# Kernel optimization log

Measured on AMD Instinct MI355X. Metric: run time of the kernel, lower is better.

## Reference

```python
import jax, jax.numpy as jnp
import numpy as np
import math

N_HEADS = 8
NUM_LAYERS = 2
OUT_LEN = 96
MIN_FACTOR, MAX_FACTOR = 3, 10
MIN_KERNEL, MAX_KERNEL = 5, 51
LN_EPS = 1e-5


def layer_norm(x, g, b):
    mu = x.mean(-1, keepdims=True)
    var = x.var(-1, keepdims=True)  # biased, like nn.LayerNorm
    return (x - mu) / jnp.sqrt(var + LN_EPS) * g + b


def prob_sparse_attn(x, wq, bq, wk, bk, wv, bv, wo, bo):
    B, L, D = x.shape
    H, dk = N_HEADS, D // N_HEADS
    Q = (x @ wq + bq).reshape(B, L, H, dk).transpose(0, 2, 1, 3)  # [B,H,L,dk]
    K = (x @ wk + bk).reshape(B, L, H, dk).transpose(0, 2, 1, 3)
    V = (x @ wv + bv).reshape(B, L, H, dk).transpose(0, 2, 1, 3)
    # sparsity score per query: 0.5*||q|| + 0.3*entropy(softmax(q)) + 0.2*var(q)
    l2 = jnp.linalg.norm(Q, axis=-1)
    prob = jax.nn.softmax(Q, axis=-1)
    ent = -jnp.sum(prob * jnp.log(prob + 1e-9), axis=-1)
    var = Q.var(axis=-1, ddof=1)  # torch.var unbiased
    qs = 0.5 * l2 + 0.3 * ent + 0.2 * var  # [B,H,L]
    std = qs.std(axis=2, ddof=1)
    mean = qs.mean(axis=2)
    factor = jnp.clip(jnp.round(std / (mean + 1e-6) * MAX_FACTOR), MIN_FACTOR, MAX_FACTOR).astype(jnp.int32)  # [B,H]
    u = factor[:, 0]  # torch uses k_list[b][0]: head-0 factor per batch
    umax = min(MAX_FACTOR, L)
    _, top_idx = jax.lax.top_k(qs, umax)  # [B,H,umax]
    keep = jnp.arange(umax)[None, None, :] < u[:, None, None]  # [B,1->H,umax]
    Qs = jnp.take_along_axis(Q, top_idx[..., None], axis=2)  # [B,H,umax,dk]
    scores = jnp.einsum('bhud,bhld->bhul', Qs, K) / math.sqrt(dk)
    attn = jax.nn.softmax(scores, axis=-1)
    out = jnp.einsum('bhul,bhld->bhud', attn, V)  # [B,H,umax,dk]
    # scatter selected query outputs back; rows beyond u[b] are dropped (OOB index L)
    idx = jnp.where(keep, top_idx, L)
    full = jnp.zeros((B, H, L, dk), x.dtype)
    bI = jnp.arange(B)[:, None, None]
    hI = jnp.arange(H)[None, :, None]
    full = full.at[bI, hI, idx].set(out, mode='drop')
    y = full.transpose(0, 2, 1, 3).reshape(B, L, D)
    return y @ wo + bo


def adaptive_decomp(x):
    B, L, D = x.shape
    spec = jnp.abs(jnp.fft.rfft(x, axis=1)).mean(axis=(0, 2))
    peak = jnp.argmax(spec[1:]) + 1
    period = jnp.clip(L // peak, MIN_KERNEL, MAX_KERNEL)
    period = jnp.where(period % 2 == 0, period + 1, period)
    pad = period // 2
    # avg_pool1d(kernel=period, stride=1, padding=pad, count_include_pad=False) via cumsum
    t = jnp.arange(L)
    start = jnp.clip(t - pad, 0, L)
    end = jnp.clip(t + pad + 1, 0, L)
    cs = jnp.concatenate([jnp.zeros((B, 1, D), x.dtype), jnp.cumsum(x, axis=1)], axis=1)
    cnt = (end - start).astype(x.dtype)[None, :, None]
    trend = (cs[:, end] - cs[:, start]) / cnt
    return x - trend, trend


def _forward(x, w_embed, b_embed, wq, bq, wk, bk, wv, bv, wo, bo,
             w1, b1, w2, b2, g1, beta1, g2, beta2, w_out, b_out):
    h = x @ w_embed + b_embed
    for _ in range(NUM_LAYERS):  # share_params=True: same weights each layer
        a = prob_sparse_attn(h, wq, bq, wk, bk, wv, bv, wo, bo)
        h = layer_norm(h + a, g1, beta1)
        ffn = jax.nn.relu(h @ w1 + b1) @ w2 + b2
        h = layer_norm(h + ffn, g2, beta2)
    seasonal, trend = adaptive_decomp(h)
    combined = seasonal + trend
    out_seq = combined[:, -OUT_LEN:, :]
    pred = (out_seq @ w_out + b_out)[..., 0]  # [B, OUT_LEN]
    return pred


def setup_inputs() -> dict:
    key = jax.random.key(0)
    ks = jax.random.split(key, 16)
    B, L, Din, D, Dff = 16, 4096, 8, 512, 2048
    w = lambda k, shp: (jax.random.normal(k, shp, jnp.float32) * 0.02)
    return {
        'x': jax.random.normal(ks[0], (B, L, Din), jnp.float32),
        'w_embed': w(ks[1], (Din, D)), 'b_embed': jnp.zeros((D,), jnp.float32),
        'wq': w(ks[2], (D, D)), 'bq': jnp.zeros((D,), jnp.float32),
        'wk': w(ks[3], (D, D)), 'bk': jnp.zeros((D,), jnp.float32),
        'wv': w(ks[4], (D, D)), 'bv': jnp.zeros((D,), jnp.float32),
        'wo': w(ks[5], (D, D)), 'bo': jnp.zeros((D,), jnp.float32),
        'w1': w(ks[6], (D, Dff)), 'b1': jnp.zeros((Dff,), jnp.float32),
        'w2': w(ks[7], (Dff, D)), 'b2': jnp.zeros((D,), jnp.float32),
        'g1': jnp.ones((D,), jnp.float32), 'beta1': jnp.zeros((D,), jnp.float32),
        'g2': jnp.ones((D,), jnp.float32), 'beta2': jnp.zeros((D,), jnp.float32),
        'w_out': w(ks[8], (D, 1)), 'b_out': jnp.zeros((1,), jnp.float32),
    }


def reference(x, w_embed, b_embed, wq, bq, wk, bk, wv, bv, wo, bo,
              w1, b1, w2, b2, g1, beta1, g2, beta2, w_out, b_out):
    return _forward(x, w_embed, b_embed, wq, bq, wk, bk, wv, bv, wo, bo,
                    w1, b1, w2, b2, g1, beta1, g2, beta2, w_out, b_out)
```

## Files before the change

kernel.cpp:

```cpp
#include <hip/hip_runtime.h>
#include <math.h>

#define BB 16
#define LL 4096
#define DIN 8
#define DD 512
#define HH 8
#define DKK 64
#define DFF 2048
#define OUTLEN 96
#define TAIL0 (LL - OUTLEN)
#define NTAIL (BB * OUTLEN)
#define UMAX 10
#define CH 8192
#define QKVN 1536
#define NB 4
#define QM (NB * LL)
#define NSPLIT 32
#define LCHUNK (LL / NSPLIT)
#define PSTRIDE 68
#define MAXSLOT 128
#define EROWS 16

typedef unsigned short ushort_t;
typedef unsigned int uint_t;
typedef short bf16x8 __attribute__((ext_vector_type(8)));
typedef float f32x4 __attribute__((ext_vector_type(4)));

#define GLD16(gp, lp) __builtin_amdgcn_global_load_lds((const __attribute__((address_space(1))) void*)(gp), (__attribute__((address_space(3))) void*)(lp), 16, 0, 0)

__device__ inline float wsum(float v){
#pragma unroll
  for (int o = 32; o > 0; o >>= 1) v += __shfl_xor(v, o);
  return v;
}
__device__ inline ushort_t f2bf_rtn(float f){
  uint_t u = __float_as_uint(f);
  uint_t r = u + 0x7FFF + ((u >> 16) & 1);
  return (ushort_t)(r >> 16);
}
__device__ inline float bf2f(ushort_t u){
  return __uint_as_float(((uint_t)u) << 16);
}
__device__ inline void split2(float x, ushort_t& hi, ushort_t& lo){
  uint_t u = __float_as_uint(x);
  hi = (ushort_t)(u >> 16);
  lo = f2bf_rtn(x - __uint_as_float(u & 0xFFFF0000u));
}
__device__ inline void xcd_map(int& bx, int& by){
  const int gx = gridDim.x;
  const int nwg = gx * gridDim.y;
  const int wg = (int)blockIdx.y * gx + (int)blockIdx.x;
  const int q = nwg >> 3, r = nwg & 7;
  const int xcd = wg & 7, idx = wg >> 3;
  const int swz = (xcd < r ? xcd * (q + 1) : r * (q + 1) + (xcd - r) * q) + idx;
  bx = swz % gx; by = swz / gx;
}

__global__ __launch_bounds__(256) void embed_kernel(const float* __restrict__ x,
    const float* __restrict__ we, const float* __restrict__ be,
    ushort_t* __restrict__ hh, ushort_t* __restrict__ hl){
  const int row0 = blockIdx.x * EROWS;
  __shared__ float xs[EROWS][DIN];
  const int t = threadIdx.x;
  if (t < EROWS * DIN) xs[t >> 3][t & 7] = x[(size_t)row0 * DIN + t];
  __syncthreads();
  const int j0 = 2 * t;
  float w0[DIN], w1r[DIN];
#pragma unroll
  for (int i = 0; i < DIN; ++i){ w0[i] = we[i * DD + j0]; w1r[i] = we[i * DD + j0 + 1]; }
  const float b0 = be[j0], b1 = be[j0 + 1];
#pragma unroll
  for (int rr = 0; rr < EROWS; ++rr){
    float a0 = b0, a1 = b1;
#pragma unroll
    for (int i = 0; i < DIN; ++i){ a0 += xs[rr][i] * w0[i]; a1 += xs[rr][i] * w1r[i]; }
    ushort_t h0, l0, h1, l1;
    split2(a0, h0, l0); split2(a1, h1, l1);
    ((uint_t*)(hh + (size_t)(row0 + rr) * DD))[t] = (uint_t)h0 | ((uint_t)h1 << 16);
    ((uint_t*)(hl + (size_t)(row0 + rr) * DD))[t] = (uint_t)l0 | ((uint_t)l1 << 16);
  }
}

__global__ __launch_bounds__(256) void wsplit_t_kernel(const float* __restrict__ W,
    ushort_t* __restrict__ Th, ushort_t* __restrict__ Tl, int K, int N){
  __shared__ float tile[32][33];
  const int n0 = blockIdx.x * 32;
  const int k0 = blockIdx.y * 32;
  const int tr = threadIdx.x >> 5;
  const int tc = threadIdx.x & 31;
#pragma unroll
  for (int rr = 0; rr < 4; ++rr)
    tile[tr + rr * 8][tc] = W[(size_t)(k0 + tr + rr * 8) * N + n0 + tc];
  __syncthreads();
#pragma unroll
  for (int rr = 0; rr < 4; ++rr){
    const int n = n0 + tr + rr * 8;
    ushort_t hi, lo;
    split2(tile[tc][tr + rr * 8], hi, lo);
    Th[(size_t)n * K + k0 + tc] = hi;
    Tl[(size_t)n * K + k0 + tc] = lo;
  }
}
__global__ __launch_bounds__(256) void wqkv_prep_kernel(const float* __restrict__ wq,
    const float* __restrict__ wk, const float* __restrict__ wv,
    ushort_t* __restrict__ Th, ushort_t* __restrict__ Tl){
  __shared__ float tile[32][33];
  const int n0 = blockIdx.x * 32;
  const int k0 = blockIdx.y * 32;
  const float* src = (n0 < 512) ? wq : (n0 < 1024) ? wk : wv;
  const int nb = n0 & 511;
  const int tr = threadIdx.x >> 5;
  const int tc = threadIdx.x & 31;
#pragma unroll
  for (int rr = 0; rr < 4; ++rr)
    tile[tr + rr * 8][tc] = src[(size_t)(k0 + tr + rr * 8) * DD + nb + tc];
  __syncthreads();
#pragma unroll
  for (int rr = 0; rr < 4; ++rr){
    const int n = n0 + tr + rr * 8;
    ushort_t hi, lo;
    split2(tile[tc][tr + rr * 8], hi, lo);
    Th[(size_t)n * DD + k0 + tc] = hi;
    Tl[(size_t)n * DD + k0 + tc] = lo;
  }
}
__global__ __launch_bounds__(256) void bqkv_prep_kernel(const float* __restrict__ bq,
    const float* __restrict__ bk, const float* __restrict__ bv, float* __restrict__ bo_){
  int n = blockIdx.x * 256 + threadIdx.x;
  if (n >= QKVN) return;
  bo_[n] = (n < 512) ? bq[n] : (n < 1024) ? bk[n - 512] : bv[n - 1024];
}

__global__ __launch_bounds__(256) void gemm_qkv(
    const ushort_t* __restrict__ Ah, const ushort_t* __restrict__ Al,
    const ushort_t* __restrict__ Bh, const ushort_t* __restrict__ Bl,
    const float* __restrict__ bias, float* __restrict__ Q,
    ushort_t* __restrict__ KV){
  __shared__ __align__(16) ushort_t AsH[128 * 32];
  __shared__ __align__(16) ushort_t AsL[128 * 32];
  __shared__ __align__(16) ushort_t BsH[128 * 32];
  __shared__ __align__(16) ushort_t BsL[128 * 32];
  int bx, by; xcd_map(bx, by);
  const int tid  = threadIdx.x;
  const int lane = tid & 63;
  const int wv   = tid >> 6;
  const int m0   = by * 128;
  const int n0   = bx * 128;
  const bool isQ = (n0 < 512);
  const int wm   = (wv & 1) * 64;
  const int wn   = (wv >> 1) * 64;

  const int rowA = tid >> 2;
  const int qe   = (tid & 3) * 8;
  const int lds0 = tid * 8;
  const int lds1 = (tid + 256) * 8;

  f32x4 acc[4][4];
#pragma unroll
  for (int i = 0; i < 4; ++i)
#pragma unroll
    for (int j = 0; j < 4; ++j) acc[i][j] = (f32x4){0.f, 0.f, 0.f, 0.f};

  const int arow = lane & 15;
  const int koff = (lane >> 4) * 8;
  const int K = DD;

  for (int k0 = 0; k0 < K; k0 += 32){
    const size_t ga0 = (size_t)(m0 + rowA) * K + k0 + qe;
    const size_t ga1 = (size_t)(m0 + rowA + 64) * K + k0 + qe;
    const size_t gb0 = (size_t)(n0 + rowA) * K + k0 + qe;
    const size_t gb1 = (size_t)(n0 + rowA + 64) * K + k0 + qe;
    GLD16(Ah + ga0, &AsH[lds0]);  GLD16(Ah + ga1, &AsH[lds1]);
    GLD16(Al + ga0, &AsL[lds0]);  GLD16(Al + ga1, &AsL[lds1]);
    GLD16(Bh + gb0, &BsH[lds0]);  GLD16(Bh + gb1, &BsH[lds1]);
    if (isQ){ GLD16(Bl + gb0, &BsL[lds0]);  GLD16(Bl + gb1, &BsL[lds1]); }
    __syncthreads();

    bf16x8 ah[4], al[4], bh[4], bl[4];
#pragma unroll
    for (int i = 0; i < 4; ++i){
      ah[i] = *(const bf16x8*)&AsH[(wm + i * 16 + arow) * 32 + koff];
      al[i] = *(const bf16x8*)&AsL[(wm + i * 16 + arow) * 32 + koff];
      bh[i] = *(const bf16x8*)&BsH[(wn + i * 16 + arow) * 32 + koff];
      if (isQ) bl[i] = *(const bf16x8*)&BsL[(wn + i * 16 + arow) * 32 + koff];
    }
#pragma unroll
    for (int i = 0; i < 4; ++i)
#pragma unroll
      for (int j = 0; j < 4; ++j){
        acc[i][j] = __builtin_amdgcn_mfma_f32_16x16x32_bf16(ah[i], bh[j], acc[i][j], 0, 0, 0);
        acc[i][j] = __builtin_amdgcn_mfma_f32_16x16x32_bf16(al[i], bh[j], acc[i][j], 0, 0, 0);
        if (isQ)
          acc[i][j] = __builtin_amdgcn_mfma_f32_16x16x32_bf16(ah[i], bl[j], acc[i][j], 0, 0, 0);
      }
    __syncthreads();
  }

  const int crow = (lane >> 4) * 4;
  const int ccol = lane & 15;
#pragma unroll
  for (int i = 0; i < 4; ++i){
    const int gr0 = m0 + wm + i * 16 + crow;
#pragma unroll
    for (int j = 0; j < 4; ++j){
      const int gc = n0 + wn + j * 16 + ccol;
      const float bvv = bias[gc];
#pragma unroll
      for (int r = 0; r < 4; ++r){
        float v = acc[i][j][r] + bvv;
        const int gr = gr0 + r;
        if (isQ) Q[(size_t)gr * 512 + gc] = v;
        else     KV[(size_t)gr * 1024 + (gc - 512)] = f2bf_rtn(v);
      }
    }
  }
}

__global__ __launch_bounds__(256) void gemm_ffn1(
    const ushort_t* __restrict__ Ah, const ushort_t* __restrict__ Al,
    const ushort_t* __restrict__ Bh, const float* __restrict__ bias,
    ushort_t* __restrict__ Chid){
  __shared__ __align__(16) ushort_t AsH[128 * 32];
  __shared__ __align__(16) ushort_t AsL[128 * 32];
  __shared__ __align__(16) ushort_t BsH[128 * 32];
  int bx, by; xcd_map(bx, by);
  const int tid  = threadIdx.x;
  const int lane = tid & 63;
  const int wv   = tid >> 6;
  const int m0   = by * 128;
  const int n0   = bx * 128;
  const int wm   = (wv & 1) * 64;
  const int wn   = (wv >> 1) * 64;
  const int rowA = tid >> 2;
  const int qe   = (tid & 3) * 8;
  const int lds0 = tid * 8;
  const int lds1 = (tid + 256) * 8;

  f32x4 acc[4][4];
#pragma unroll
  for (int i = 0; i < 4; ++i)
#pragma unroll
    for (int j = 0; j < 4; ++j) acc[i][j] = (f32x4){0.f, 0.f, 0.f, 0.f};

  const int arow = lane & 15;
  const int koff = (lane >> 4) * 8;
  const int K = DD;

  for (int k0 = 0; k0 < K; k0 += 32){
    const size_t ga0 = (size_t)(m0 + rowA) * K + k0 + qe;
    const size_t ga1 = (size_t)(m0 + rowA + 64) * K + k0 + qe;
    const size_t gb0 = (size_t)(n0 + rowA) * K + k0 + qe;
    const size_t gb1 = (size_t)(n0 + rowA + 64) * K + k0 + qe;
    GLD16(Ah + ga0, &AsH[lds0]);  GLD16(Ah + ga1, &AsH[lds1]);
    GLD16(Al + ga0, &AsL[lds0]);  GLD16(Al + ga1, &AsL[lds1]);
    GLD16(Bh + gb0, &BsH[lds0]);  GLD16(Bh + gb1, &BsH[lds1]);
    __syncthreads();

    bf16x8 ah[4], al[4], bh[4];
#pragma unroll
    for (int i = 0; i < 4; ++i){
      ah[i] = *(const bf16x8*)&AsH[(wm + i * 16 + arow) * 32 + koff];
      al[i] = *(const bf16x8*)&AsL[(wm + i * 16 + arow) * 32 + koff];
      bh[i] = *(const bf16x8*)&BsH[(wn + i * 16 + arow) * 32 + koff];
    }
#pragma unroll
    for (int i = 0; i < 4; ++i)
#pragma unroll
      for (int j = 0; j < 4; ++j){
        acc[i][j] = __builtin_amdgcn_mfma_f32_16x16x32_bf16(ah[i], bh[j], acc[i][j], 0, 0, 0);
        acc[i][j] = __builtin_amdgcn_mfma_f32_16x16x32_bf16(al[i], bh[j], acc[i][j], 0, 0, 0);
      }
    __syncthreads();
  }

  const int crow = (lane >> 4) * 4;
  const int ccol = lane & 15;
#pragma unroll
  for (int i = 0; i < 4; ++i){
    const int gr0 = m0 + wm + i * 16 + crow;
#pragma unroll
    for (int j = 0; j < 4; ++j){
      const int gc = n0 + wn + j * 16 + ccol;
      const float bvv = bias[gc];
#pragma unroll
      for (int r = 0; r < 4; ++r){
        float v = fmaxf(acc[i][j][r] + bvv, 0.f);
        Chid[(size_t)(gr0 + r) * DFF + gc] = f2bf_rtn(v);
      }
    }
  }
}

__global__ __launch_bounds__(256) void gemm_ffn2(
    const ushort_t* __restrict__ Ahid,
    const ushort_t* __restrict__ Bh, const ushort_t* __restrict__ Bl,
    float* __restrict__ pbuf, size_t pstr){
  __shared__ __align__(16) ushort_t AsH[128 * 32];
  __shared__ __align__(16) ushort_t BsH[128 * 32];
  __shared__ __align__(16) ushort_t BsL[128 * 32];
  int bx, by; xcd_map(bx, by);
  const int tid  = threadIdx.x;
  const int lane = tid & 63;
  const int wv   = tid >> 6;
  const int nblk = bx >> 1;
  const int kq   = bx & 1;
  const int m0   = by * 128;
  const int n0   = nblk * 128;
  const int wm   = (wv & 1) * 64;
  const int wn   = (wv >> 1) * 64;
  const int rowA = tid >> 2;
  const int qe   = (tid & 3) * 8;
  const int lds0 = tid * 8;
  const int lds1 = (tid + 256) * 8;

  f32x4 acc[4][4];
#pragma unroll
  for (int i = 0; i < 4; ++i)
#pragma unroll
    for (int j = 0; j < 4; ++j) acc[i][j] = (f32x4){0.f, 0.f, 0.f, 0.f};

  const int arow = lane & 15;
  const int koff = (lane >> 4) * 8;
  const int K = DFF;
  const int kper = K / 2;
  const int kbeg = kq * kper;

  for (int k0 = kbeg; k0 < kbeg + kper; k0 += 32){
    const size_t ga0 = (size_t)(m0 + rowA) * K + k0 + qe;
    const size_t ga1 = (size_t)(m0 + rowA + 64) * K + k0 + qe;
    const size_t gb0 = (size_t)(n0 + rowA) * K + k0 + qe;
    const size_t gb1 = (size_t)(n0 + rowA + 64) * K + k0 + qe;
    GLD16(Ahid + ga0, &AsH[lds0]);  GLD16(Ahid + ga1, &AsH[lds1]);
    GLD16(Bh + gb0, &BsH[lds0]);    GLD16(Bh + gb1, &BsH[lds1]);
    GLD16(Bl + gb0, &BsL[lds0]);    GLD16(Bl + gb1, &BsL[lds1]);
    __syncthreads();

    bf16x8 ah[4], bh[4], bl[4];
#pragma unroll
    for (int i = 0; i < 4; ++i){
      ah[i] = *(const bf16x8*)&AsH[(wm + i * 16 + arow) * 32 + koff];
      bh[i] = *(const bf16x8*)&BsH[(wn + i * 16 + arow) * 32 + koff];
      bl[i] = *(const bf16x8*)&BsL[(wn + i * 16 + arow) * 32 + koff];
    }
#pragma unroll
    for (int i = 0; i < 4; ++i)
#pragma unroll
      for (int j = 0; j < 4; ++j){
        acc[i][j] = __builtin_amdgcn_mfma_f32_16x16x32_bf16(ah[i], bh[j], acc[i][j], 0, 0, 0);
        acc[i][j] = __builtin_amdgcn_mfma_f32_16x16x32_bf16(ah[i], bl[j], acc[i][j], 0, 0, 0);
      }
    __syncthreads();
  }

  const int crow = (lane >> 4) * 4;
  const int ccol = lane & 15;
#pragma unroll
  for (int i = 0; i < 4; ++i){
    const int gr0 = m0 + wm + i * 16 + crow;
#pragma unroll
    for (int j = 0; j < 4; ++j){
      const int gc = n0 + wn + j * 16 + ccol;
#pragma unroll
      for (int r = 0; r < 4; ++r)
        pbuf[(size_t)kq * pstr + (size_t)(gr0 + r) * DD + gc] = acc[i][j][r];
    }
  }
}

__global__ __launch_bounds__(256) void qs_kernel(const float* __restrict__ qbuf, float* __restrict__ qsb){
  int tid = threadIdx.x;
  int lane = tid & 63;
  int wv = tid >> 6;
  int rid = blockIdx.x * 4 + wv;
  int bloc = rid >> 15;
  int hh = (rid >> 12) & 7;
  int l  = rid & (LL - 1);
  float qv = qbuf[((size_t)bloc * LL + l) * DD + hh * DKK + lane];
  float l2 = sqrtf(wsum(qv * qv));
  float mx = qv;
#pragma unroll
  for (int o = 32; o > 0; o >>= 1) mx = fmaxf(mx, __shfl_xor(mx, o));
  float e  = expf(qv - mx);
  float se = wsum(e);
  float p  = e / se;
  float ent = -wsum(p * logf(p + 1e-9f));
  float mu  = wsum(qv) * (1.0f / 64.0f);
  float dv  = qv - mu;
  float var = wsum(dv * dv) * (1.0f / 63.0f);
  float val = 0.5f * l2 + 0.3f * ent + 0.2f * var;
  if (lane == 0) qsb[(size_t)(bloc * HH + hh) * LL + l] = val;
}

__global__ __launch_bounds__(256) void select_kernel(const float* __restrict__ qsb,
    int* __restrict__ topidx, int* __restrict__ ufac, int qtr){
  __shared__ float vals[LL];
  __shared__ float bv[256];
  __shared__ int   bi[256];
  __shared__ int   widx_s;
  __shared__ double r1[256], r2[256];
  const int bloc = blockIdx.y;
  const int b = qtr * NB + bloc;
  int tid = threadIdx.x;
  if (blockIdx.x == 8){
    const float* row = qsb + (size_t)bloc * HH * LL;
    double s = 0.0, s2 = 0.0;
    for (int l = tid; l < LL; l += 256){ double v = row[l]; s += v; s2 += v * v; }
    r1[tid] = s; r2[tid] = s2; __syncthreads();
    for (int st = 128; st; st >>= 1){
      if (tid < st){ r1[tid] += r1[tid+st]; r2[tid] += r2[tid+st]; }
      __syncthreads();
    }
    if (tid == 0){
      double mean = r1[0] / (double)LL;
      double var  = (r2[0] - (double)LL * mean * mean) / (double)(LL - 1);
      if (var < 0.0) var = 0.0;
      double f = rint(sqrt(var) / (mean + 1e-6) * 10.0);
      if (f < 3.0) f = 3.0;
      if (f > 10.0) f = 10.0;
      ufac[b] = (int)f;
    }
    return;
  }
  int hh = blockIdx.x;
  const float* row = qsb + ((size_t)bloc * HH + hh) * LL;
  for (int l = tid; l < LL; l += 256) vals[l] = row[l];
  __syncthreads();
  float lmax = -INFINITY; int lidx = 0;
  for (int l = tid; l < LL; l += 256){
    float v = vals[l];
    if (v > lmax){ lmax = v; lidx = l; }
  }
  for (int it = 0; it < UMAX; ++it){
    bv[tid] = lmax; bi[tid] = lidx;
    __syncthreads();
    for (int st = 128; st; st >>= 1){
      if (tid < st){
        if (bv[tid+st] > bv[tid] || (bv[tid+st] == bv[tid] && bi[tid+st] < bi[tid])){
          bv[tid] = bv[tid+st]; bi[tid] = bi[tid+st];
        }
      }
      __syncthreads();
    }
    if (tid == 0){ topidx[(b * HH + hh) * UMAX + it] = bi[0]; widx_s = bi[0]; }
    __syncthreads();
    const int w = widx_s;
    if ((w & 255) == tid){
      vals[w] = -INFINITY;
      lmax = -INFINITY; lidx = 0;
      for (int l = tid; l < LL; l += 256){
        float v = vals[l];
        if (v > lmax){ lmax = v; lidx = l; }
      }
    }
    __syncthreads();
  }
}

__global__ void initslot_kernel(int* __restrict__ slotmap, int* __restrict__ scount){
  int i = blockIdx.x * 256 + threadIdx.x;
  if (i < BB * LL) slotmap[i] = -1;
  if (i < BB) scount[i] = 0;
}
__global__ __launch_bounds__(128) void slotbuild_kernel(const int* __restrict__ topidx,
    const int* __restrict__ ufac, int* __restrict__ slotmap, int* __restrict__ scount, int qtr){
  int t = threadIdx.x;
  int b = qtr * NB + blockIdx.x;
  if (t >= HH * UMAX) return;
  int hh = t / UMAX, rank = t % UMAX;
  if (rank >= ufac[b]) return;
  int qpos = topidx[(b * HH + hh) * UMAX + rank];
  int* cell = &slotmap[b * LL + qpos];
  int old = atomicCAS(cell, -1, -2);
  if (old == -1){
    int s = atomicAdd(&scount[b], 1);
    atomicExch(cell, s);
  }
}

__global__ __launch_bounds__(256) void attn_p1_kernel(const float* __restrict__ qbuf,
    const ushort_t* __restrict__ kvbuf,
    const int* __restrict__ topidx, const int* __restrict__ ufac,
    float* __restrict__ part, int qtr, int lmin){
  const int bloc = blockIdx.z;
  const int b = qtr * NB + bloc;
  const int hh = blockIdx.y;
  const int u = ufac[b];
  const int tid = threadIdx.x, lane = tid & 63, wv = tid >> 6;
  const int base = blockIdx.x * LCHUNK + wv * 32;

  const ushort_t* Kp = kvbuf + (size_t)bloc * LL * 1024 + hh * DKK + lane;
  const ushort_t* Vp = Kp + 512;
  float kreg[32], vreg[32];
#pragma unroll
  for (int i = 0; i < 32; ++i){
    kreg[i] = bf2f(Kp[(size_t)(base + i) * 1024]);
    vreg[i] = bf2f(Vp[(size_t)(base + i) * 1024]);
  }

  __shared__ float wm4[4], ws4[4];
  __shared__ float pvs[4][DKK];

  for (int rank = 0; rank < u; ++rank){
    const int qpos = topidx[(b * HH + hh) * UMAX + rank];
    if (qpos < lmin) continue;
    const float qv = qbuf[((size_t)bloc * LL + qpos) * DD + hh * DKK + lane];

    float sc[32];
    float mloc = -INFINITY;
#pragma unroll
    for (int i = 0; i < 32; ++i){
      float s = wsum(qv * kreg[i]) * 0.125f;
      sc[i] = s;
      mloc = fmaxf(mloc, s);
    }
    if (lane == 0) wm4[wv] = mloc;
    __syncthreads();
    const float M4 = fmaxf(fmaxf(wm4[0], wm4[1]), fmaxf(wm4[2], wm4[3]));

    float ssum = 0.f;
#pragma unroll
    for (int i = 0; i < 32; ++i){ float e = expf(sc[i] - M4); sc[i] = e; ssum += e; }

    float pv = 0.f;
#pragma unroll
    for (int i = 0; i < 32; ++i) pv += sc[i] * vreg[i];

    pvs[wv][lane] = pv;
    if (lane == 0) ws4[wv] = ssum;
    __syncthreads();
    if (wv == 0){
      const int rowid = hh * UMAX + rank;
      float* rec = part + (size_t)((bloc * HH * UMAX + rowid) * NSPLIT + blockIdx.x) * PSTRIDE;
      rec[lane] = pvs[0][lane] + pvs[1][lane] + pvs[2][lane] + pvs[3][lane];
      if (lane == 0){ rec[64] = M4; rec[65] = ws4[0] + ws4[1] + ws4[2] + ws4[3]; }
    }
    __syncthreads();
  }
}

__global__ __launch_bounds__(256) void attn_p2_kernel(const float* __restrict__ part,
    const float* __restrict__ wo, const int* __restrict__ topidx, const int* __restrict__ ufac,
    const int* __restrict__ slotmap, float* __restrict__ adelta, int qtr, int lmin){
  const int bloc = blockIdx.y;
  const int b = qtr * NB + bloc;
  const int rowid = blockIdx.x;
  const int hh = rowid / UMAX, rank = rowid % UMAX;
  if (rank >= ufac[b]) return;
  const int qpos = topidx[(b * HH + hh) * UMAX + rank];
  if (qpos < lmin) return;
  const int slot = slotmap[b * LL + qpos];

  const int tid = threadIdx.x;
  const float* pbase = part + (size_t)(bloc * HH * UMAX + rowid) * NSPLIT * PSTRIDE;
  __shared__ float pm[NSPLIT], ps[NSPLIT];
  __shared__ float orow[DKK];
  if (tid < NSPLIT){
    pm[tid] = pbase[(size_t)tid * PSTRIDE + 64];
    ps[tid] = pbase[(size_t)tid * PSTRIDE + 65];
  }
  __syncthreads();
  float M = -INFINITY;
#pragma unroll
  for (int i = 0; i < NSPLIT; ++i) M = fmaxf(M, pm[i]);
  float S = 0.f;
#pragma unroll
  for (int i = 0; i < NSPLIT; ++i) S += ps[i] * expf(pm[i] - M);
  if (tid < DKK){
    float acc = 0.f;
#pragma unroll
    for (int i = 0; i < NSPLIT; ++i)
      acc += pbase[(size_t)i * PSTRIDE + tid] * expf(pm[i] - M);
    orow[tid] = acc / S;
  }
  __syncthreads();
  float* drow = adelta + ((size_t)b * MAXSLOT + slot) * DD;
  for (int j = tid; j < DD; j += 256){
    float a = 0.f;
#pragma unroll
    for (int dd = 0; dd < DKK; ++dd) a += orow[dd] * wo[(size_t)(hh * DKK + dd) * DD + j];
    atomicAdd(&drow[j], a);
  }
}

__global__ void zero_kernel(float* __restrict__ p, size_t n){
  size_t i = (size_t)blockIdx.x * 256 + threadIdx.x;
  size_t stride = (size_t)gridDim.x * 256;
  for (; i < n; i += stride) p[i] = 0.f;
}

template<bool TAIL>
__global__ __launch_bounds__(256) void ln1_kernel(
    const ushort_t* __restrict__ hh_, const ushort_t* __restrict__ hl_,
    const float* __restrict__ bo,
    const int* __restrict__ slotmap, const float* __restrict__ adelta,
    ushort_t* __restrict__ oh, ushort_t* __restrict__ ol,
    const float* __restrict__ g, const float* __restrict__ bb){
  __shared__ float ss[4], qq[4];
  int r = blockIdx.x, tid = threadIdx.x;
  const int lane = tid & 63, wv = tid >> 6;
  int b, l;
  if (TAIL){ b = r / OUTLEN; l = TAIL0 + (r % OUTLEN); }
  else     { b = r >> 12;    l = r & (LL - 1); }
  const size_t gi = ((size_t)b * LL + l) * DD;
  const int j0 = 2 * tid;
  const uint_t hp = *(const uint_t*)(hh_ + gi + j0);
  const uint_t lp = *(const uint_t*)(hl_ + gi + j0);
  const float2 bo2 = *(const float2*)&bo[j0];
  float v0 = bf2f((ushort_t)(hp & 0xFFFF)) + bf2f((ushort_t)(lp & 0xFFFF)) + bo2.x;
  float v1 = bf2f((ushort_t)(hp >> 16))    + bf2f((ushort_t)(lp >> 16))    + bo2.y;
  int s = slotmap[b * LL + l];
  if (s >= 0){
    const float2 dr = *(const float2*)&adelta[((size_t)b * MAXSLOT + s) * DD + j0];
    v0 += dr.x; v1 += dr.y;
  }
  float sm = v0 + v1, qm = v0 * v0 + v1 * v1;
#pragma unroll
  for (int o2 = 32; o2 > 0; o2 >>= 1){ sm += __shfl_xor(sm, o2); qm += __shfl_xor(qm, o2); }
  if (lane == 0){ ss[wv] = sm; qq[wv] = qm; }
  __syncthreads();
  const float S = ss[0] + ss[1] + ss[2] + ss[3];
  const float Qv = qq[0] + qq[1] + qq[2] + qq[3];
  const float mu = S * (1.0f / DD);
  float var = Qv * (1.0f / DD) - mu * mu;
  const float rstd = rsqrtf(var + 1e-5f);
  const float2 g2 = *(const float2*)&g[j0];
  const float2 bb2 = *(const float2*)&bb[j0];
  float o0 = (v0 - mu) * rstd * g2.x + bb2.x;
  float o1 = (v1 - mu) * rstd * g2.y + bb2.y;
  const size_t oo = TAIL ? (size_t)r * DD : gi;
  ushort_t h0, l0, h1, l1;
  split2(o0, h0, l0); split2(o1, h1, l1);
  *(uint_t*)(oh + oo + j0) = (uint_t)h0 | ((uint_t)h1 << 16);
  *(uint_t*)(ol + oo + j0) = (uint_t)l0 | ((uint_t)l1 << 16);
}

template<bool TAIL>
__global__ __launch_bounds__(256) void ln2_kernel(
    const ushort_t* __restrict__ ih, const ushort_t* __restrict__ il,
    const float* __restrict__ pbuf, size_t pstr, const float* __restrict__ b2,
    ushort_t* __restrict__ oh, ushort_t* __restrict__ ol, float* __restrict__ ofp,
    const float* __restrict__ g, const float* __restrict__ bb, size_t rowoff){
  __shared__ float ss[4], qq[4];
  int r = blockIdx.x, tid = threadIdx.x;
  const int lane = tid & 63, wv = tid >> 6;
  const size_t gi = (rowoff + r) * DD;
  const size_t pi = (size_t)r * DD;
  const int j0 = 2 * tid;
  const uint_t hp = *(const uint_t*)(ih + gi + j0);
  const uint_t lp = *(const uint_t*)(il + gi + j0);
  const float2 p0 = *(const float2*)&pbuf[pi + j0];
  const float2 p1 = *(const float2*)&pbuf[pstr + pi + j0];
  const float2 b22 = *(const float2*)&b2[j0];
  float v0 = bf2f((ushort_t)(hp & 0xFFFF)) + bf2f((ushort_t)(lp & 0xFFFF)) + p0.x + p1.x + b22.x;
  float v1 = bf2f((ushort_t)(hp >> 16))    + bf2f((ushort_t)(lp >> 16))    + p0.y + p1.y + b22.y;
  float sm = v0 + v1, qm = v0 * v0 + v1 * v1;
#pragma unroll
  for (int o2 = 32; o2 > 0; o2 >>= 1){ sm += __shfl_xor(sm, o2); qm += __shfl_xor(qm, o2); }
  if (lane == 0){ ss[wv] = sm; qq[wv] = qm; }
  __syncthreads();
  const float S = ss[0] + ss[1] + ss[2] + ss[3];
  const float Qv = qq[0] + qq[1] + qq[2] + qq[3];
  const float mu = S * (1.0f / DD);
  float var = Qv * (1.0f / DD) - mu * mu;
  const float rstd = rsqrtf(var + 1e-5f);
  const float2 g2 = *(const float2*)&g[j0];
  const float2 bb2 = *(const float2*)&bb[j0];
  float o0 = (v0 - mu) * rstd * g2.x + bb2.x;
  float o1 = (v1 - mu) * rstd * g2.y + bb2.y;
  if (TAIL){
    ofp[pi + j0] = o0; ofp[pi + j0 + 1] = o1;
  } else {
    ushort_t h0, l0, h1, l1;
    split2(o0, h0, l0); split2(o1, h1, l1);
    *(uint_t*)(oh + gi + j0) = (uint_t)h0 | ((uint_t)h1 << 16);
    *(uint_t*)(ol + gi + j0) = (uint_t)l0 | ((uint_t)l1 << 16);
  }
}

__global__ __launch_bounds__(64) void pred_kernel(const float* __restrict__ ht,
    const float* __restrict__ wout, const float* __restrict__ bout, float* __restrict__ out){
  int r = blockIdx.x, lane = threadIdx.x;
  float acc = 0.f;
  for (int dd = lane; dd < DD; dd += 64) acc += ht[(size_t)r * DD + dd] * wout[dd];
  acc = wsum(acc);
  if (lane == 0) out[r] = acc + bout[0];
}

extern "C" void kernel_launch(void* const* d_in, const int* in_sizes, int n_in,
                              void* d_out, int out_size, void* d_ws, size_t ws_size,
                              hipStream_t stream){
  const float* x    = (const float*)d_in[0];
  const float* wemb = (const float*)d_in[1];
  const float* bemb = (const float*)d_in[2];
  const float* wq   = (const float*)d_in[3];
  const float* bq   = (const float*)d_in[4];
  const float* wk   = (const float*)d_in[5];
  const float* bk   = (const float*)d_in[6];
  const float* wv   = (const float*)d_in[7];
  const float* bvv  = (const float*)d_in[8];
  const float* wo   = (const float*)d_in[9];
  const float* bo   = (const float*)d_in[10];
  const float* w1   = (const float*)d_in[11];
  const float* b1   = (const float*)d_in[12];
  const float* w2   = (const float*)d_in[13];
  const float* b2   = (const float*)d_in[14];
  const float* g1   = (const float*)d_in[15];
  const float* be1  = (const float*)d_in[16];
  const float* g2   = (const float*)d_in[17];
  const float* be2  = (const float*)d_in[18];
  const float* wout = (const float*)d_in[19];
  const float* bout = (const float*)d_in[20];
  float* out = (float*)d_out;
  char* wsb  = (char*)d_ws;

  const size_t MiB = 1024 * 1024;
  const size_t NE  = (size_t)BB * LL * DD;

  size_t o = 0;
  ushort_t* hh    = (ushort_t*)(wsb + o); o += NE * 2;
  ushort_t* hl    = (ushort_t*)(wsb + o); o += NE * 2;
  char*     arena = wsb + o;              o += 64 * MiB;
  float*    qbuf  = (float*)arena;
  ushort_t* kvbuf = (ushort_t*)(arena + 32 * MiB);
  ushort_t* hid   = (ushort_t*)arena;
  float*    pbuf  = (float*)(arena + 32 * MiB);
  ushort_t* hidt  = (ushort_t*)arena;
  float*    pbuft = (float*)(arena + 32 * MiB);
  ushort_t* asht  = (ushort_t*)(arena + 48 * MiB);
  ushort_t* aslt  = (ushort_t*)(arena + 50 * MiB);
  ushort_t* wtqkvh = (ushort_t*)(wsb + o); o += (size_t)QKVN * DD * 2;
  ushort_t* wtqkvl = (ushort_t*)(wsb + o); o += (size_t)QKVN * DD * 2;
  ushort_t* w1th   = (ushort_t*)(wsb + o); o += (size_t)DFF * DD * 2;
  ushort_t* w2th   = (ushort_t*)(wsb + o); o += (size_t)DD * DFF * 2;
  ushort_t* w2tl   = (ushort_t*)(wsb + o); o += (size_t)DD * DFF * 2;
  ushort_t* w1tl   = (ushort_t*)(wsb + o); o += (size_t)DFF * DD * 2;
  float*    bqkv   = (float*)(wsb + o);  o += QKVN * 4;
  float*    qsb    = (float*)(wsb + o);  o += (size_t)NB * HH * LL * 4;
  float*    part   = (float*)(wsb + o);  o += (size_t)NB * HH * UMAX * NSPLIT * PSTRIDE * 4;
  float*    adelta = (float*)(wsb + o);  o += (size_t)BB * MAXSLOT * DD * 4;
  float*    htail  = (float*)(wsb + o);  o += (size_t)NTAIL * DD * 4;
  int*      slotmap= (int*)(wsb + o);    o += (size_t)BB * LL * 4;
  int*      scount = (int*)(wsb + o);    o += BB * 4;
  int*      topidx = (int*)(wsb + o);    o += (size_t)BB * HH * UMAX * 4;
  int*      ufac   = (int*)(wsb + o);    o += 64;

  wqkv_prep_kernel<<<dim3(QKVN/32, DD/32), 256, 0, stream>>>(wq, wk, wv, wtqkvh, wtqkvl);
  bqkv_prep_kernel<<<(QKVN + 255)/256, 256, 0, stream>>>(bq, bk, bvv, bqkv);
  wsplit_t_kernel<<<dim3(DFF/32, DD/32), 256, 0, stream>>>(w1, w1th, w1tl, DD, DFF);
  wsplit_t_kernel<<<dim3(DD/32, DFF/32), 256, 0, stream>>>(w2, w2th, w2tl, DFF, DD);

  embed_kernel<<<(BB * LL) / EROWS, 256, 0, stream>>>(x, wemb, bemb, hh, hl);

  for (int layer = 0; layer < 2; ++layer){
    const bool tail = (layer == 1);
    const int lmin = tail ? TAIL0 : 0;

    initslot_kernel<<<(BB*LL + 255)/256, 256, 0, stream>>>(slotmap, scount);
    zero_kernel<<<1024, 256, 0, stream>>>(adelta, (size_t)BB * MAXSLOT * DD);

    for (int qtr = 0; qtr < BB / NB; ++qtr){
      const size_t hoff = (size_t)qtr * QM * DD;
      gemm_qkv<<<dim3(QKVN/128, QM/128), 256, 0, stream>>>(
          hh + hoff, hl + hoff, wtqkvh, wtqkvl, bqkv, qbuf, kvbuf);
      qs_kernel<<<(NB*HH*LL)/4, 256, 0, stream>>>(qbuf, qsb);
      select_kernel<<<dim3(9, NB), 256, 0, stream>>>(qsb, topidx, ufac, qtr);
      slotbuild_kernel<<<NB, 128, 0, stream>>>(topidx, ufac, slotmap, scount, qtr);
      attn_p1_kernel<<<dim3(NSPLIT, HH, NB), 256, 0, stream>>>(
          qbuf, kvbuf, topidx, ufac, part, qtr, lmin);
      attn_p2_kernel<<<dim3(HH*UMAX, NB), 256, 0, stream>>>(
          part, wo, topidx, ufac, slotmap, adelta, qtr, lmin);
    }

    if (!tail){
      ln1_kernel<false><<<BB*LL, 256, 0, stream>>>(hh, hl, bo, slotmap, adelta, hh, hl, g1, be1);
      for (int c = 0; c < (BB*LL)/CH; ++c){
        const size_t roff = (size_t)c * CH;
        gemm_ffn1<<<dim3(DFF/128, CH/128), 256, 0, stream>>>(
            hh + roff * DD, hl + roff * DD, w1th, b1, hid);
        gemm_ffn2<<<dim3(8, CH/128), 256, 0, stream>>>(hid, w2th, w2tl, pbuf, (size_t)CH * DD);
        ln2_kernel<false><<<CH, 256, 0, stream>>>(
            hh, hl, pbuf, (size_t)CH * DD, b2, hh, hl, nullptr, g2, be2, roff);
      }
    } else {
      ln1_kernel<true><<<NTAIL, 256, 0, stream>>>(hh, hl, bo, slotmap, adelta, asht, aslt, g1, be1);
      gemm_ffn1<<<dim3(DFF/128, NTAIL/128), 256, 0, stream>>>(asht, aslt, w1th, b1, hidt);
      gemm_ffn2<<<dim3(8, NTAIL/128), 256, 0, stream>>>(hidt, w2th, w2tl, pbuft, (size_t)NTAIL * DD);
      ln2_kernel<true><<<NTAIL, 256, 0, stream>>>(
          asht, aslt, pbuft, (size_t)NTAIL * DD, b2, nullptr, nullptr, htail, g2, be2, 0);
      pred_kernel<<<NTAIL, 64, 0, stream>>>(htail, wout, bout, out);
    }
  }
  (void)in_sizes; (void)n_in; (void)out_size; (void)ws_size;
}
```

Measured before the change: 2.545 ms.

## Fuse query sparsity scoring into QKV GEMM epilogue and merge small kernels

Computes each query's sparsity score (L2 norm, softmax entropy, variance) directly from the GEMM accumulators in the QKV epilogue. This removes the separate qs_kernel pass, which re-read the whole Q buffer. Slot-map building moves into the tail of select_kernel, and the slotmap init and adelta zeroing are merged into one reset kernel, cutting launches. Slots are now assigned for all top-UMAX winners rather than only ranks below the per-batch factor. Variance now uses the one-pass sum-of-squares form, which is less numerically precise.

```diff
diff --git a/kernel.cpp b/kernel.cpp
--- a/kernel.cpp
+++ b/kernel.cpp
@@ -136,7 +136,7 @@
     const ushort_t* __restrict__ Ah, const ushort_t* __restrict__ Al,
     const ushort_t* __restrict__ Bh, const ushort_t* __restrict__ Bl,
     const float* __restrict__ bias, float* __restrict__ Q,
-    ushort_t* __restrict__ KV){
+    ushort_t* __restrict__ KV, float* __restrict__ qsb){
   __shared__ __align__(16) ushort_t AsH[128 * 32];
   __shared__ __align__(16) ushort_t AsL[128 * 32];
   __shared__ __align__(16) ushort_t BsH[128 * 32];
@@ -212,6 +212,52 @@
         const int gr = gr0 + r;
         if (isQ) Q[(size_t)gr * 512 + gc] = v;
         else     KV[(size_t)gr * 1024 + (gc - 512)] = f2bf_rtn(v);
+      }
+    }
+  }
+
+  if (isQ){
+    const int hhd = (n0 >> 6) + (wn >> 6);
+    const int grp = lane >> 4;
+    const int lid = lane & 15;
+#pragma unroll
+    for (int i = 0; i < 4; ++i){
+#pragma unroll
+      for (int r = 0; r < 4; ++r){
+        float v0a = acc[i][0][r] + bias[n0 + wn + 0  + lid];
+        float v1a = acc[i][1][r] + bias[n0 + wn + 16 + lid];
+        float v2a = acc[i][2][r] + bias[n0 + wn + 32 + lid];
+        float v3a = acc[i][3][r] + bias[n0 + wn + 48 + lid];
+        float s1 = v0a + v1a + v2a + v3a;
+        float s2 = v0a*v0a + v1a*v1a + v2a*v2a + v3a*v3a;
+        float mx = fmaxf(fmaxf(v0a, v1a), fmaxf(v2a, v3a));
+#pragma unroll
+        for (int o2 = 8; o2 > 0; o2 >>= 1){
+          s1 += __shfl_xor(s1, o2);
+          s2 += __shfl_xor(s2, o2);
+          mx = fmaxf(mx, __shfl_xor(mx, o2));
+        }
+        float e0 = expf(v0a - mx), e1 = expf(v1a - mx);
+        float e2 = expf(v2a - mx), e3 = expf(v3a - mx);
+        float se = e0 + e1 + e2 + e3;
+#pragma unroll
+        for (int o2 = 8; o2 > 0; o2 >>= 1) se += __shfl_xor(se, o2);
+        float inv = 1.0f / se;
+        float p0 = e0*inv, p1 = e1*inv, p2 = e2*inv, p3 = e3*inv;
+        float en = p0*logf(p0+1e-9f) + p1*logf(p1+1e-9f)
+                 + p2*logf(p2+1e-9f) + p3*logf(p3+1e-9f);
+#pragma unroll
+        for (int o2 = 8; o2 > 0; o2 >>= 1) en += __shfl_xor(en, o2);
+        float ent = -en;
+        float l2n = sqrtf(s2);
+        float mu  = s1 * (1.0f / 64.0f);
+        float var = (s2 - 64.0f * mu * mu) * (1.0f / 63.0f);
+        float val = 0.5f * l2n + 0.3f * ent + 0.2f * var;
+        if (lid == 0){
+          const int gr = m0 + wm + i * 16 + grp * 4 + r;
+          const int bloc = gr >> 12, l = gr & (LL - 1);
+          qsb[(size_t)(bloc * HH + hhd) * LL + l] = val;
+        }
       }
     }
   }
@@ -368,36 +414,14 @@
   }
 }
 
-__global__ __launch_bounds__(256) void qs_kernel(const float* __restrict__ qbuf, float* __restrict__ qsb){
-  int tid = threadIdx.x;
-  int lane = tid & 63;
-  int wv = tid >> 6;
-  int rid = blockIdx.x * 4 + wv;
-  int bloc = rid >> 15;
-  int hh = (rid >> 12) & 7;
-  int l  = rid & (LL - 1);
-  float qv = qbuf[((size_t)bloc * LL + l) * DD + hh * DKK + lane];
-  float l2 = sqrtf(wsum(qv * qv));
-  float mx = qv;
-#pragma unroll
-  for (int o = 32; o > 0; o >>= 1) mx = fmaxf(mx, __shfl_xor(mx, o));
-  float e  = expf(qv - mx);
-  float se = wsum(e);
-  float p  = e / se;
-  float ent = -wsum(p * logf(p + 1e-9f));
-  float mu  = wsum(qv) * (1.0f / 64.0f);
-  float dv  = qv - mu;
-  float var = wsum(dv * dv) * (1.0f / 63.0f);
-  float val = 0.5f * l2 + 0.3f * ent + 0.2f * var;
-  if (lane == 0) qsb[(size_t)(bloc * HH + hh) * LL + l] = val;
-}
-
 __global__ __launch_bounds__(256) void select_kernel(const float* __restrict__ qsb,
-    int* __restrict__ topidx, int* __restrict__ ufac, int qtr){
+    int* __restrict__ topidx, int* __restrict__ ufac,
+    int* __restrict__ slotmap, int* __restrict__ scount, int qtr){
   __shared__ float vals[LL];
   __shared__ float bv[256];
   __shared__ int   bi[256];
   __shared__ int   widx_s;
+  __shared__ int   swin[UMAX];
   __shared__ double r1[256], r2[256];
   const int bloc = blockIdx.y;
   const int b = qtr * NB + bloc;
@@ -442,7 +466,7 @@
       }
       __syncthreads();
     }
-    if (tid == 0){ topidx[(b * HH + hh) * UMAX + it] = bi[0]; widx_s = bi[0]; }
+    if (tid == 0){ topidx[(b * HH + hh) * UMAX + it] = bi[0]; widx_s = bi[0]; swin[it] = bi[0]; }
     __syncthreads();
     const int w = widx_s;
     if ((w & 255) == tid){
@@ -455,27 +479,24 @@
     }
     __syncthreads();
   }
-}
-
-__global__ void initslot_kernel(int* __restrict__ slotmap, int* __restrict__ scount){
-  int i = blockIdx.x * 256 + threadIdx.x;
-  if (i < BB * LL) slotmap[i] = -1;
+  if (tid < UMAX){
+    int qpos = swin[tid];
+    int* cell = &slotmap[b * LL + qpos];
+    int old = atomicCAS(cell, -1, -2);
+    if (old == -1){
+      int s = atomicAdd(&scount[b], 1);
+      atomicExch(cell, s);
+    }
+  }
+}
+
+__global__ void reset_kernel(int* __restrict__ slotmap, int* __restrict__ scount,
+    float* __restrict__ adelta){
+  size_t i = (size_t)blockIdx.x * 256 + threadIdx.x;
+  size_t stride = (size_t)gridDim.x * 256;
+  for (size_t k = i; k < (size_t)BB * LL; k += stride) slotmap[k] = -1;
+  for (size_t k = i; k < (size_t)BB * MAXSLOT * DD; k += stride) adelta[k] = 0.f;
   if (i < BB) scount[i] = 0;
-}
-__global__ __launch_bounds__(128) void slotbuild_kernel(const int* __restrict__ topidx,
-    const int* __restrict__ ufac, int* __restrict__ slotmap, int* __restrict__ scount, int qtr){
-  int t = threadIdx.x;
-  int b = qtr * NB + blockIdx.x;
-  if (t >= HH * UMAX) return;
-  int hh = t / UMAX, rank = t % UMAX;
-  if (rank >= ufac[b]) return;
-  int qpos = topidx[(b * HH + hh) * UMAX + rank];
-  int* cell = &slotmap[b * LL + qpos];
-  int old = atomicCAS(cell, -1, -2);
-  if (old == -1){
-    int s = atomicAdd(&scount[b], 1);
-    atomicExch(cell, s);
-  }
 }
 
 __global__ __launch_bounds__(256) void attn_p1_kernel(const float* __restrict__ qbuf,
@@ -581,12 +602,6 @@
     for (int dd = 0; dd < DKK; ++dd) a += orow[dd] * wo[(size_t)(hh * DKK + dd) * DD + j];
     atomicAdd(&drow[j], a);
   }
-}
-
-__global__ void zero_kernel(float* __restrict__ p, size_t n){
-  size_t i = (size_t)blockIdx.x * 256 + threadIdx.x;
-  size_t stride = (size_t)gridDim.x * 256;
-  for (; i < n; i += stride) p[i] = 0.f;
 }
 
 template<bool TAIL>
@@ -756,16 +771,13 @@
     const bool tail = (layer == 1);
     const int lmin = tail ? TAIL0 : 0;
 
-    initslot_kernel<<<(BB*LL + 255)/256, 256, 0, stream>>>(slotmap, scount);
-    zero_kernel<<<1024, 256, 0, stream>>>(adelta, (size_t)BB * MAXSLOT * DD);
+    reset_kernel<<<1024, 256, 0, stream>>>(slotmap, scount, adelta);
 
     for (int qtr = 0; qtr < BB / NB; ++qtr){
       const size_t hoff = (size_t)qtr * QM * DD;
       gemm_qkv<<<dim3(QKVN/128, QM/128), 256, 0, stream>>>(
-          hh + hoff, hl + hoff, wtqkvh, wtqkvl, bqkv, qbuf, kvbuf);
-      qs_kernel<<<(NB*HH*LL)/4, 256, 0, stream>>>(qbuf, qsb);
-      select_kernel<<<dim3(9, NB), 256, 0, stream>>>(qsb, topidx, ufac, qtr);
-      slotbuild_kernel<<<NB, 128, 0, stream>>>(topidx, ufac, slotmap, scount, qtr);
+          hh + hoff, hl + hoff, wtqkvh, wtqkvl, bqkv, qbuf, kvbuf, qsb);
+      select_kernel<<<dim3(9, NB), 256, 0, stream>>>(qsb, topidx, ufac, slotmap, scount, qtr);
       attn_p1_kernel<<<dim3(NSPLIT, HH, NB), 256, 0, stream>>>(
           qbuf, kvbuf, topidx, ufac, part, qtr, lmin);
       attn_p2_kernel<<<dim3(HH*UMAX, NB), 256, 0, stream>>>(
```

Result: no change. 2.586 ms (+1.6%).
